# Optimization experiments

Hardware: AMD Instinct MI355X
Metric: run time of the kernel (lower is better)

Reference implementation:

```python
import jax, jax.numpy as jnp
import numpy as np

B, OP, MA, F_IN, F_OUT = 8, 400, 200, 64, 64


def setup_inputs() -> dict:
    key = jax.random.key(0)
    ks = jax.random.split(key, 8)
    x = jax.random.normal(ks[0], (B, OP, F_IN), dtype=jnp.float32)
    y = jax.random.normal(ks[1], (B, MA, F_IN), dtype=jnp.float32)
    z = jax.random.normal(ks[2], (B, OP, MA, F_IN), dtype=jnp.float32)
    op_ma_adj = jax.random.randint(ks[3], (B, OP, MA), 0, 2, dtype=jnp.int32)
    # xavier-uniform-ish params
    lim = float(np.sqrt(6.0 / (F_IN + F_OUT)))
    W_op = jax.random.uniform(ks[4], (F_IN, F_OUT), minval=-lim, maxval=lim, dtype=jnp.float32)
    W_ma = jax.random.uniform(ks[5], (F_IN, F_OUT), minval=-lim, maxval=lim, dtype=jnp.float32)
    W_edge = jax.random.uniform(ks[6], (F_IN, F_OUT), minval=-lim, maxval=lim, dtype=jnp.float32)
    lim_a = float(np.sqrt(6.0 / (1 + 3 * F_OUT)))
    att_vec = jax.random.uniform(ks[7], (3 * F_OUT,), minval=-lim_a, maxval=lim_a, dtype=jnp.float32)
    return {"x": x, "y": y, "z": z, "op_ma_adj": op_ma_adj,
            "W_op": W_op, "W_ma": W_ma, "W_edge": W_edge, "att_vec": att_vec}


def reference(x, y, z, op_ma_adj, W_op, W_ma, W_edge, att_vec):
    F = W_op.shape[1]
    h_op = jnp.einsum('bni,io->bno', x, W_op)                      # [B, op, F]
    h = jnp.einsum('bmi,io->bmo', y, W_ma)                         # [B, ma, F]
    h_edge = jnp.einsum('bnmi,io->bnmo', z, W_edge).transpose(0, 2, 1, 3)  # [B, ma, op, F]
    # attention score: concat([h_op, h_ma, h_edge]) @ a  ==  per-part dot products (no BxMAxOPx3F materialization)
    a_op, a_ma, a_edge = att_vec[:F], att_vec[F:2 * F], att_vec[2 * F:]
    e = (jnp.einsum('bnf,f->bn', h_op, a_op)[:, None, :]
         + jnp.einsum('bmf,f->bm', h, a_ma)[:, :, None]
         + jnp.einsum('bmnf,f->bmn', h_edge, a_edge))              # [B, ma, op]
    e = jax.nn.leaky_relu(e, negative_slope=0.01)
    adjT = op_ma_adj.transpose(0, 2, 1)                            # [B, ma, op]
    row_empty = jnp.all(adjT == 0, axis=-1, keepdims=True)         # [B, ma, 1]
    att = jnp.where(adjT > 0, e, -jnp.inf)
    att = jnp.where(row_empty, 0.0, att)                           # empty rows -> uniform softmax (matches torch)
    att = jax.nn.softmax(att, axis=-1)                             # [B, ma, op]
    h_op_edge = h_op[:, None, :, :] + h_edge                       # [B, ma, op, F]
    h_prime = jnp.einsum('bmn,bmnf->bmf', att, h_op_edge)          # [B, ma, F]
    h_prime = jnp.where(row_empty, 0.0, h_prime) + h
    return jax.nn.elu(h_prime)
```

## Files before the change

### kernel.cpp

```cpp
#include <hip/hip_runtime.h>
#include <math.h>

#define B_   8
#define OP_  400
#define MA_  200
#define NCH  4
#define CH   100
#define RPW  25
#define PSTR 132
#define NEGM -1.0e30f

__global__ __launch_bounds__(256) void precompute_k(
    const float* __restrict__ x, const float* __restrict__ y,
    const float* __restrict__ Wop, const float* __restrict__ Wma,
    const float* __restrict__ Wedge, const float* __restrict__ att,
    float* __restrict__ ws_we, float* __restrict__ ws_eop, float* __restrict__ ws_ema)
{
    __shared__ float w_s[192];
    const int tid = threadIdx.x, wv = tid >> 6, ln = tid & 63;
    if (tid < 192) {
        const int which = tid >> 6, i = tid & 63;
        const float* W = (which == 0) ? Wop : ((which == 1) ? Wma : Wedge);
        const float* a = att + which * 64;
        float acc = 0.f;
        #pragma unroll 8
        for (int f = 0; f < 64; ++f) acc = fmaf(W[i * 64 + f], a[f], acc);
        w_s[tid] = acc;
    }
    __syncthreads();
    if (blockIdx.x == 0 && tid < 64) ws_we[tid] = w_s[128 + tid];

    const int row = blockIdx.x * 4 + wv;
    if (row < B_ * OP_) {
        float s = x[(size_t)row * 64 + ln] * w_s[ln];
        #pragma unroll
        for (int o = 32; o > 0; o >>= 1) s += __shfl_xor(s, o, 64);
        if (ln == 0) ws_eop[row] = s;
    } else if (row < B_ * OP_ + B_ * MA_) {
        const int r2 = row - B_ * OP_;
        float s = y[(size_t)r2 * 64 + ln] * w_s[64 + ln];
        #pragma unroll
        for (int o = 32; o > 0; o >>= 1) s += __shfl_xor(s, o, 64);
        if (ln == 0) ws_ema[r2] = s;
    }
}

__global__ __launch_bounds__(256) void gat_chunk(
    const float* __restrict__ x, const float* __restrict__ z,
    const int* __restrict__ adj,
    const float* __restrict__ ws_we, const float* __restrict__ ws_eop,
    const float* __restrict__ ws_ema, float* __restrict__ part)
{
    __shared__ float we_s[64];
    __shared__ float s_arr[CH];
    __shared__ float red[8];
    __shared__ float vred[4][64];
    __shared__ float ured[4][64];

    const int tid = threadIdx.x, wv = tid >> 6, ln = tid & 63;
    const int blk = blockIdx.x;
    const int bm = blk / NCH, c = blk % NCH;
    const int b = bm / MA_, m = bm % MA_;
    const int n0 = c * CH;
    const int nbase = wv * RPW;

    if (tid < 64) we_s[tid] = ws_we[tid];
    __syncthreads();

    const float* zb = z + ((size_t)(b * OP_ + n0) * MA_ + m) * 64;
    float zreg[RPW];
    #pragma unroll
    for (int i = 0; i < RPW; ++i)
        zreg[i] = zb[(size_t)(nbase + i) * (MA_ * 64) + ln];

    #pragma unroll
    for (int i = 0; i < RPW; ++i) {
        float s = zreg[i] * we_s[ln];
        #pragma unroll
        for (int o = 32; o > 0; o >>= 1) s += __shfl_xor(s, o, 64);
        if (ln == 0) s_arr[nbase + i] = s;
    }
    __syncthreads();

    const float ema = ws_ema[bm];
    if (tid < CH) {
        const int n = n0 + tid;
        float e = s_arr[tid] + ws_eop[b * OP_ + n] + ema;
        e = (e >= 0.f) ? e : 0.01f * e;
        const int ad = adj[((size_t)(b * OP_ + n)) * MA_ + m];
        s_arr[tid] = (ad != 0) ? e : NEGM;
    }
    __syncthreads();

    float lm = NEGM;
    for (int n = tid; n < CH; n += 256) lm = fmaxf(lm, s_arr[n]);
    #pragma unroll
    for (int o = 32; o > 0; o >>= 1) lm = fmaxf(lm, __shfl_xor(lm, o, 64));
    if (ln == 0) red[wv] = lm;
    __syncthreads();
    const float M = fmaxf(fmaxf(red[0], red[1]), fmaxf(red[2], red[3]));

    float ls = 0.f;
    for (int n = tid; n < CH; n += 256) {
        const float sv = s_arr[n];
        const float p = (sv > -1.0e29f) ? __expf(sv - M) : 0.f;
        s_arr[n] = p;
        ls += p;
    }
    #pragma unroll
    for (int o = 32; o > 0; o >>= 1) ls += __shfl_xor(ls, o, 64);
    if (ln == 0) red[4 + wv] = ls;
    __syncthreads();
    const float L = red[4] + red[5] + red[6] + red[7];

    const float* xb = x + (size_t)(b * OP_ + n0) * 64;
    float v = 0.f, u = 0.f;
    #pragma unroll
    for (int i = 0; i < RPW; ++i) {
        const float p = s_arr[nbase + i];
        v = fmaf(p, zreg[i], v);
        u = fmaf(p, xb[(size_t)(nbase + i) * 64 + ln], u);
    }
    vred[wv][ln] = v; ured[wv][ln] = u;
    __syncthreads();

    float* pp = part + (size_t)blk * PSTR;
    if (tid < 64)        pp[tid]      = vred[0][tid] + vred[1][tid] + vred[2][tid] + vred[3][tid];
    else if (tid < 128)  pp[tid]      = ured[0][tid-64] + ured[1][tid-64] + ured[2][tid-64] + ured[3][tid-64];
    else if (tid == 128) { pp[128] = M; pp[129] = L; }
}

__global__ __launch_bounds__(256) void gat_combine(
    const float* __restrict__ y,
    const float* __restrict__ Wop, const float* __restrict__ Wma,
    const float* __restrict__ Wedge,
    const float* __restrict__ part, float* __restrict__ out)
{
    __shared__ float vs[4][64], us[4][64], ys[4][64];
    const int tid = threadIdx.x, wv = tid >> 6, ln = tid & 63;
    const int row = blockIdx.x * 4 + wv;

    const float* pp = part + (size_t)row * NCH * PSTR;
    float M = NEGM;
    #pragma unroll
    for (int c = 0; c < NCH; ++c) M = fmaxf(M, pp[c * PSTR + 128]);
    float L = 0.f, v = 0.f, u = 0.f;
    #pragma unroll
    for (int c = 0; c < NCH; ++c) {
        const float Mc = pp[c * PSTR + 128];
        const float w  = (Mc > -1.0e29f) ? __expf(Mc - M) : 0.f;
        L += w * pp[c * PSTR + 129];
        v += w * pp[c * PSTR + ln];
        u += w * pp[c * PSTR + 64 + ln];
    }
    const float inv = (L > 0.f) ? (1.f / L) : 0.f;
    vs[wv][ln] = v * inv;
    us[wv][ln] = u * inv;
    ys[wv][ln] = y[(size_t)row * 64 + ln];
    __syncthreads();

    float hv = 0.f;
    #pragma unroll 8
    for (int i = 0; i < 64; ++i) {
        hv += vs[wv][i] * Wedge[i * 64 + ln]
            + us[wv][i] * Wop[i * 64 + ln]
            + ys[wv][i] * Wma[i * 64 + ln];
    }
    out[(size_t)row * 64 + ln] = (hv > 0.f) ? hv : (__expf(hv) - 1.f);
}

extern "C" void kernel_launch(void* const* d_in, const int* in_sizes, int n_in,
                              void* d_out, int out_size, void* d_ws, size_t ws_size,
                              hipStream_t stream) {
    const float* x     = (const float*)d_in[0];
    const float* y     = (const float*)d_in[1];
    const float* z     = (const float*)d_in[2];
    const int*   adj   = (const int*)d_in[3];
    const float* Wop   = (const float*)d_in[4];
    const float* Wma   = (const float*)d_in[5];
    const float* Wedge = (const float*)d_in[6];
    const float* att   = (const float*)d_in[7];

    float* ws     = (float*)d_ws;
    float* ws_we  = ws;
    float* ws_eop = ws + 64;
    float* ws_ema = ws + 64 + B_ * OP_;
    float* part   = ws + 64 + B_ * OP_ + B_ * MA_;

    precompute_k<<<1200, 256, 0, stream>>>(
        x, y, Wop, Wma, Wedge, att, ws_we, ws_eop, ws_ema);
    gat_chunk<<<B_ * MA_ * NCH, 256, 0, stream>>>(
        x, z, adj, ws_we, ws_eop, ws_ema, part);
    gat_combine<<<(B_ * MA_) / 4, 256, 0, stream>>>(
        y, Wop, Wma, Wedge, part, (float*)d_out);
}
```

Before: 271.9 us.

## Tile z over op-chunk by ma-range with contiguous float4 loads into shared memory

Replaces the per-(b,m) chunk kernel with a tile kernel. Each block covers 10 op rows by 20 ma columns and loads the contiguous z rows via float4 into padded shared memory. The edge scores are computed per thread with a serial dot product, and each wave then does a small softmax partial per ma column. This targets the strided, poorly coalesced 256-byte z gathers of the old layout and removes the cross-wave reductions. In exchange there are 40 partials per row for the combine step, which enlarges the workspace and the combine loop, and shared memory use rises to about 57KB per block, which may limit occupancy.

```diff
diff --git a/kernel.cpp b/kernel.cpp
--- a/kernel.cpp
+++ b/kernel.cpp
@@ -4,10 +4,11 @@
 #define B_   8
 #define OP_  400
 #define MA_  200
-#define NCH  4
-#define CH   100
-#define RPW  25
-#define PSTR 132
+#define CN   10
+#define MT   20
+#define NCH  40
+#define NMT  10
+#define PSTR 130
 #define NEGM -1.0e30f
 
 __global__ __launch_bounds__(256) void precompute_k(
@@ -45,89 +46,79 @@
     }
 }
 
-__global__ __launch_bounds__(256) void gat_chunk(
+__global__ __launch_bounds__(256) void gat_tile(
     const float* __restrict__ x, const float* __restrict__ z,
     const int* __restrict__ adj,
     const float* __restrict__ ws_we, const float* __restrict__ ws_eop,
     const float* __restrict__ ws_ema, float* __restrict__ part)
 {
-    __shared__ float we_s[64];
-    __shared__ float s_arr[CH];
-    __shared__ float red[8];
-    __shared__ float vred[4][64];
-    __shared__ float ured[4][64];
+    __shared__ float4 z4[200 * 17];
+    __shared__ float  sc[200];
+    __shared__ float  xt[CN * 64];
+    __shared__ float  we_s[64];
+    __shared__ float  eop_s[CN];
+    __shared__ float  ema_s[MT];
+    __shared__ int    adj_s[200];
+
+    const float* zf = (const float*)z4;
 
     const int tid = threadIdx.x, wv = tid >> 6, ln = tid & 63;
-    const int blk = blockIdx.x;
-    const int bm = blk / NCH, c = blk % NCH;
-    const int b = bm / MA_, m = bm % MA_;
-    const int n0 = c * CH;
-    const int nbase = wv * RPW;
+    const int bid = blockIdx.x;
+    const int mt = bid % NMT;
+    const int ch = (bid / NMT) % NCH;
+    const int b  = bid / (NMT * NCH);
+    const int n0 = ch * CN, m0 = mt * MT;
 
-    if (tid < 64) we_s[tid] = ws_we[tid];
+    for (int c = tid; c < CN * MT * 16; c += 256) {
+        const int i = c / (MT * 16);
+        const int r = c % (MT * 16);
+        const int j = r / 16;
+        const int k = r % 16;
+        const float* zs = z + (((size_t)(b * OP_ + n0 + i)) * MA_ + m0) * 64;
+        z4[(i * MT + j) * 17 + k] = *(const float4*)(zs + r * 4);
+    }
+    for (int c = tid; c < CN * 64; c += 256)
+        xt[c] = x[((size_t)(b * OP_ + n0 + (c >> 6))) * 64 + (c & 63)];
+    if (tid < 200)
+        adj_s[tid] = adj[((size_t)(b * OP_ + n0 + tid / MT)) * MA_ + m0 + tid % MT];
+    else if (tid < 200 + 50) {
+        const int t = tid - 200;
+        if (t < CN)            eop_s[t]      = ws_eop[b * OP_ + n0 + t];
+        else if (t < CN + MT)  ema_s[t - CN] = ws_ema[b * MA_ + m0 + (t - CN)];
+    }
+    if (tid >= 192 && tid < 256) we_s[tid - 192] = ws_we[tid - 192];
     __syncthreads();
 
-    const float* zb = z + ((size_t)(b * OP_ + n0) * MA_ + m) * 64;
-    float zreg[RPW];
-    #pragma unroll
-    for (int i = 0; i < RPW; ++i)
-        zreg[i] = zb[(size_t)(nbase + i) * (MA_ * 64) + ln];
-
-    #pragma unroll
-    for (int i = 0; i < RPW; ++i) {
-        float s = zreg[i] * we_s[ln];
-        #pragma unroll
-        for (int o = 32; o > 0; o >>= 1) s += __shfl_xor(s, o, 64);
-        if (ln == 0) s_arr[nbase + i] = s;
+    if (tid < 200) {
+        const float* zr = zf + tid * 68;
+        float s = 0.f;
+        #pragma unroll 16
+        for (int f = 0; f < 64; ++f) s = fmaf(zr[f], we_s[f], s);
+        const int i = tid / MT, j = tid % MT;
+        float e = s + eop_s[i] + ema_s[j];
+        e = (e >= 0.f) ? e : 0.01f * e;
+        sc[tid] = (adj_s[tid] != 0) ? e : NEGM;
     }
     __syncthreads();
 
-    const float ema = ws_ema[bm];
-    if (tid < CH) {
-        const int n = n0 + tid;
-        float e = s_arr[tid] + ws_eop[b * OP_ + n] + ema;
-        e = (e >= 0.f) ? e : 0.01f * e;
-        const int ad = adj[((size_t)(b * OP_ + n)) * MA_ + m];
-        s_arr[tid] = (ad != 0) ? e : NEGM;
+    for (int j = wv; j < MT; j += 4) {
+        float sv[CN];
+        float M = NEGM;
+        #pragma unroll
+        for (int i = 0; i < CN; ++i) { sv[i] = sc[i * MT + j]; M = fmaxf(M, sv[i]); }
+        float L = 0.f, v = 0.f, u = 0.f;
+        #pragma unroll
+        for (int i = 0; i < CN; ++i) {
+            const float p = (sv[i] > -1.0e29f) ? __expf(sv[i] - M) : 0.f;
+            L += p;
+            v = fmaf(p, zf[(i * MT + j) * 68 + ln], v);
+            u = fmaf(p, xt[i * 64 + ln], u);
+        }
+        float* pp = part + ((size_t)((b * MA_ + m0 + j) * NCH + ch)) * PSTR;
+        pp[ln]      = v;
+        pp[64 + ln] = u;
+        if (ln == 0) { pp[128] = M; pp[129] = L; }
     }
-    __syncthreads();
-
-    float lm = NEGM;
-    for (int n = tid; n < CH; n += 256) lm = fmaxf(lm, s_arr[n]);
-    #pragma unroll
-    for (int o = 32; o > 0; o >>= 1) lm = fmaxf(lm, __shfl_xor(lm, o, 64));
-    if (ln == 0) red[wv] = lm;
-    __syncthreads();
-    const float M = fmaxf(fmaxf(red[0], red[1]), fmaxf(red[2], red[3]));
-
-    float ls = 0.f;
-    for (int n = tid; n < CH; n += 256) {
-        const float sv = s_arr[n];
-        const float p = (sv > -1.0e29f) ? __expf(sv - M) : 0.f;
-        s_arr[n] = p;
-        ls += p;
-    }
-    #pragma unroll
-    for (int o = 32; o > 0; o >>= 1) ls += __shfl_xor(ls, o, 64);
-    if (ln == 0) red[4 + wv] = ls;
-    __syncthreads();
-    const float L = red[4] + red[5] + red[6] + red[7];
-
-    const float* xb = x + (size_t)(b * OP_ + n0) * 64;
-    float v = 0.f, u = 0.f;
-    #pragma unroll
-    for (int i = 0; i < RPW; ++i) {
-        const float p = s_arr[nbase + i];
-        v = fmaf(p, zreg[i], v);
-        u = fmaf(p, xb[(size_t)(nbase + i) * 64 + ln], u);
-    }
-    vred[wv][ln] = v; ured[wv][ln] = u;
-    __syncthreads();
-
-    float* pp = part + (size_t)blk * PSTR;
-    if (tid < 64)        pp[tid]      = vred[0][tid] + vred[1][tid] + vred[2][tid] + vred[3][tid];
-    else if (tid < 128)  pp[tid]      = ured[0][tid-64] + ured[1][tid-64] + ured[2][tid-64] + ured[3][tid-64];
-    else if (tid == 128) { pp[128] = M; pp[129] = L; }
 }
 
 __global__ __launch_bounds__(256) void gat_combine(
@@ -142,10 +133,9 @@
 
     const float* pp = part + (size_t)row * NCH * PSTR;
     float M = NEGM;
-    #pragma unroll
     for (int c = 0; c < NCH; ++c) M = fmaxf(M, pp[c * PSTR + 128]);
     float L = 0.f, v = 0.f, u = 0.f;
-    #pragma unroll
+    #pragma unroll 4
     for (int c = 0; c < NCH; ++c) {
         const float Mc = pp[c * PSTR + 128];
         const float w  = (Mc > -1.0e29f) ? __expf(Mc - M) : 0.f;
@@ -185,11 +175,11 @@
     float* ws_we  = ws;
     float* ws_eop = ws + 64;
     float* ws_ema = ws + 64 + B_ * OP_;
-    float* part   = ws + 64 + B_ * OP_ + B_ * MA_;
+    float* part   = ws + 4864;
 
     precompute_k<<<1200, 256, 0, stream>>>(
         x, y, Wop, Wma, Wedge, att, ws_we, ws_eop, ws_ema);
-    gat_chunk<<<B_ * MA_ * NCH, 256, 0, stream>>>(
+    gat_tile<<<B_ * NCH * NMT, 256, 0, stream>>>(
         x, z, adj, ws_we, ws_eop, ws_ema, part);
     gat_combine<<<(B_ * MA_) / 4, 256, 0, stream>>>(
         y, Wop, Wma, Wedge, part, (float*)d_out);
```

Result: slower. 313.2 us (+15.2%).
